# Kernel optimization log

Measured on AMD Instinct MI355X. Metric: run time of the kernel, lower is better.

Reference implementation:

```python
import jax, jax.numpy as jnp
import numpy as np

B, N, IN_F, OUT_F = 8, 2048, 256, 256
ALPHA = 0.2  # LeakyReLU negative slope
NEG_INF = -1e9


def setup_inputs() -> dict:
    key = jax.random.key(0)
    ks = jax.random.split(key, 8)
    h = jax.random.normal(ks[0], (B, N, IN_F), dtype=jnp.float32)
    adj = jax.random.randint(ks[1], (B, N, N), 0, 2, dtype=jnp.int32)
    # xavier-ish scaled params
    W_w = jax.random.normal(ks[2], (OUT_F, IN_F), dtype=jnp.float32) * (1.414 / np.sqrt(IN_F + OUT_F))
    W_b = jnp.zeros((OUT_F,), dtype=jnp.float32)
    ai_w = jax.random.normal(ks[3], (1, OUT_F), dtype=jnp.float32) * (1.414 / np.sqrt(OUT_F + 1))
    ai_b = jnp.zeros((1,), dtype=jnp.float32)
    aj_w = jax.random.normal(ks[4], (1, OUT_F), dtype=jnp.float32) * (1.414 / np.sqrt(OUT_F + 1))
    aj_b = jnp.zeros((1,), dtype=jnp.float32)
    return {"h": h, "adj": adj, "W_w": W_w, "W_b": W_b,
            "ai_w": ai_w, "ai_b": ai_b, "aj_w": aj_w, "aj_b": aj_b}


def reference(h, adj, W_w, W_b, ai_w, ai_b, aj_w, aj_b):
    # Wh: [B, N, F]
    Wh = jnp.einsum('bni,oi->bno', h, W_w) + W_b
    # additive attention scores (pos_embed_dim == 1 so the .view is a transpose)
    Wh1 = jnp.einsum('bnf,of->bno', Wh, ai_w) + ai_b        # [B, N, 1]
    Wh2 = jnp.einsum('bnf,of->bno', Wh, aj_w) + aj_b        # [B, N, 1]
    e = Wh1 + jnp.swapaxes(Wh2, 1, 2)                       # [B, N, N]
    e = jnp.where(e >= 0, e, ALPHA * e)                     # LeakyReLU
    attention = jnp.where(adj > 0, e, NEG_INF)
    attention = jax.nn.softmax(attention, axis=2)
    # dropout: inference mode (training=False) -> identity
    h_hat = jnp.einsum('bnm,bmf->bnf', attention, Wh)
    return jax.nn.elu(h_hat)  # concat=True
```

## Files before the change

### kernel.cpp

```cpp
#include <hip/hip_runtime.h>

typedef __bf16 bf16;
typedef _Float16 f16;
typedef __bf16 bf16x8 __attribute__((ext_vector_type(8)));
typedef _Float16 f16x8 __attribute__((ext_vector_type(8)));
typedef float  f32x4  __attribute__((ext_vector_type(4)));

#define B_  8
#define N_  2048
#define F_  256
#define NTOK (B_ * N_)
#define NW   (F_ * F_)
static constexpr float LOG2E = 1.44269504088896f;

__device__ __forceinline__ int detect_bf16(const void* h) {
    const unsigned* hw = (const unsigned*)h;
    unsigned w = hw[threadIdx.x & 63];
    unsigned ex = (w >> 7) & 0xFFu;
    unsigned long long b = __ballot(ex > 100u && ex < 150u);
    return __popcll(b) >= 40;
}

__device__ __forceinline__ float ldf(const void* p, int i, int isb) {
    return isb ? (float)((const bf16*)p)[i] : ((const float*)p)[i];
}


__global__ __launch_bounds__(256)
void k_cvt(const void* __restrict__ hv, const void* __restrict__ Wv,
           bf16* __restrict__ hb, bf16* __restrict__ Wb) {
    if (detect_bf16(hv)) return;
    size_t base = ((size_t)blockIdx.x * 256 + threadIdx.x) * 8;
    {
        const float* src = (const float*)hv + base;
        float4 a = *(const float4*)src;
        float4 b = *(const float4*)(src + 4);
        bf16x8 r;
        r[0]=(bf16)a.x; r[1]=(bf16)a.y; r[2]=(bf16)a.z; r[3]=(bf16)a.w;
        r[4]=(bf16)b.x; r[5]=(bf16)b.y; r[6]=(bf16)b.z; r[7]=(bf16)b.w;
        *(bf16x8*)(hb + base) = r;
    }
    if (base < NW) {
        const float* src = (const float*)Wv + base;
        float4 a = *(const float4*)src;
        float4 b = *(const float4*)(src + 4);
        bf16x8 r;
        r[0]=(bf16)a.x; r[1]=(bf16)a.y; r[2]=(bf16)a.z; r[3]=(bf16)a.w;
        r[4]=(bf16)b.x; r[5]=(bf16)b.y; r[6]=(bf16)b.z; r[7]=(bf16)b.w;
        *(bf16x8*)(Wb + base) = r;
    }
}

__global__ __launch_bounds__(256)
void k_wht(const void* __restrict__ hv, const void* __restrict__ Wv,
           const bf16* __restrict__ hcv, const bf16* __restrict__ Wcv,
           const void* __restrict__ Wbv, const void* __restrict__ ai_wv,
           const void* __restrict__ ai_bv, const void* __restrict__ aj_wv,
           const void* __restrict__ aj_bv, bf16* __restrict__ WhT2,
           unsigned* __restrict__ adjw) {
    int isb = detect_bf16(hv);
    const bf16* hb = isb ? (const bf16*)hv : hcv;
    const bf16* Wb = isb ? (const bf16*)Wv : Wcv;
    int ttile = blockIdx.x;
    int fg = threadIdx.x >> 6;
    int lane = threadIdx.x & 63;
    int T0 = ttile * 16;
    int m = lane & 15, quad = lane >> 4;

    __shared__ bf16 stage[F_ * 24];
    __shared__ float sred[4][16], tred[4][16];

    f32x4 acc[4];
#pragma unroll
    for (int ft = 0; ft < 4; ++ft) acc[ft] = (f32x4){0.f, 0.f, 0.f, 0.f};

    const bf16* hp = hb + (size_t)(T0 + m) * F_ + quad * 8;
    const bf16* wp = Wb + (size_t)(fg * 64 + m) * F_ + quad * 8;
#pragma unroll
    for (int kk = 0; kk < F_; kk += 32) {
        bf16x8 hf = *(const bf16x8*)(hp + kk);
#pragma unroll
        for (int ft = 0; ft < 4; ++ft) {
            bf16x8 wf = *(const bf16x8*)(wp + (size_t)ft * 16 * F_ + kk);
            acc[ft] = __builtin_amdgcn_mfma_f32_16x16x32_bf16(wf, hf, acc[ft], 0, 0, 0);
        }
    }
    float s_p = 0.f, t_p = 0.f;
#pragma unroll
    for (int ft = 0; ft < 4; ++ft)
#pragma unroll
        for (int r = 0; r < 4; ++r) {
            int f = fg * 64 + ft * 16 + quad * 4 + r;
            float v = acc[ft][r] + ldf(Wbv, f, isb);
            bf16 vb = (bf16)v;
            stage[f * 24 + m] = vb;
            float vr = (float)vb;
            s_p += vr * ldf(ai_wv, f, isb);
            t_p += vr * ldf(aj_wv, f, isb);
        }
    s_p += __shfl_down(s_p, 32, 64); s_p += __shfl_down(s_p, 16, 64);
    t_p += __shfl_down(t_p, 32, 64); t_p += __shfl_down(t_p, 16, 64);
    if (lane < 16) { sred[fg][lane] = s_p; tred[fg][lane] = t_p; }
    __syncthreads();

    {
        int f = threadIdx.x;
        bf16x8 pk0 = *(const bf16x8*)(stage + f * 24);
        bf16x8 pk1 = *(const bf16x8*)(stage + f * 24 + 8);
        int b  = T0 >> 11;
        int n0 = T0 & (N_ - 1);
        int jc = n0 >> 6;
        int s0 = (n0 >> 3) & 7;
        char* rowp = (char*)WhT2 + ((size_t)(b * 32 + jc) * F_ + f) * 128;
        *(bf16x8*)(rowp + (size_t)((s0)     ^ (f & 7)) * 16) = pk0;
        *(bf16x8*)(rowp + (size_t)((s0 + 1) ^ (f & 7)) * 16) = pk1;
    }

    if (threadIdx.x < 16) {
        int tid = threadIdx.x;
        int tok = T0 + tid;
        float ss = (sred[0][tid] + sred[1][tid] + sred[2][tid] + sred[3][tid]
                    + ldf(ai_bv, 0, isb)) * LOG2E;
        float tt = (tred[0][tid] + tred[1][tid] + tred[2][tid] + tred[3][tid]
                    + ldf(aj_bv, 0, isb)) * LOG2E;
        f16 th = (f16)tt, sh = (f16)ss;
        unsigned short tu, su;
        __builtin_memcpy(&tu, &th, 2);
        __builtin_memcpy(&su, &sh, 2);
        unsigned w0 = adjw[tok];
        adjw[tok] = (w0 & 0xFFFFu) | ((unsigned)tu << 16);
        unsigned w1 = adjw[NTOK + tok];
        adjw[NTOK + tok] = (w1 & 0xFFFFu) | ((unsigned)su << 16);
    }
}

__device__ __forceinline__ unsigned char pbits(uint4 a, uint4 b) {
    return (unsigned char)((a.x & 1u) | ((a.y & 1u) << 1) | ((a.z & 1u) << 2) |
                           ((a.w & 1u) << 3) | ((b.x & 1u) << 4) |
                           ((b.y & 1u) << 5) | ((b.z & 1u) << 6) |
                           ((b.w & 1u) << 7));
}

__device__ __forceinline__ void stageB(const bf16* tile, char* dst,
                                       int w, int lane) {
#pragma unroll
    for (int r = 0; r < 8; ++r) {
        int off = (w * 8 + r) * 1024;
        const bf16* g = tile + off / 2 + lane * 8;
        __builtin_amdgcn_global_load_lds(
            (const __attribute__((address_space(1))) unsigned*)g,
            (__attribute__((address_space(3))) unsigned*)(dst + off),
            16, 0, 0);
    }
}

__global__ __launch_bounds__(256, 4)
void k_attn(const unsigned* __restrict__ adjw, const bf16* __restrict__ WhT2,
            const void* __restrict__ hv, void* __restrict__ outv) {
    int isb = detect_bf16(hv);
    int bid = blockIdx.x;
    int b = bid & 7, itile = bid >> 3, i0 = itile * 32;
    int tid = threadIdx.x;
    int w = tid >> 6, lane = tid & 63, m = lane & 15, q = lane >> 4;
    int mt = w >> 1, jh = w & 1;

    __shared__ __align__(16) char smem[37376];
    char* Bbuf  = smem;
    f16* tLDS   = (f16*)(smem + 32768);
    unsigned char* pack0 = (unsigned char*)(smem + 36864);
    unsigned char* pack1 = (unsigned char*)(smem + 37120);
    float* red  = (float*)smem;

    const bf16* batch_tiles = WhT2 + ((size_t)b * 32) * F_ * 64;

#pragma unroll
    for (int k = 0; k < 8; ++k) {
        int idx = k * 256 + tid;
        unsigned wv = adjw[b * N_ + idx];
        unsigned short us = (unsigned short)(wv >> 16);
        f16 tv; __builtin_memcpy(&tv, &us, 2);
        tLDS[idx] = tv;
    }
    int row = i0 + mt * 16 + m;
    unsigned swd = adjw[NTOK + b * N_ + row];
    unsigned short su = (unsigned short)(swd >> 16);
    f16 sh; __builtin_memcpy(&sh, &su, 2);
    float s2i = (float)sh;

    int prow = tid >> 3, ps = tid & 7;
    const unsigned* arow = adjw + ((size_t)(b * N_ + i0 + prow)) * N_ + ps * 8;
    {
        uint4 x0 = *(const uint4*)arow, x1 = *(const uint4*)(arow + 4);
        pack0[prow * 8 + ps] = pbits(x0, x1);
    }
    __syncthreads();

    bf16x8 ones;
#pragma unroll
    for (int k = 0; k < 8; ++k) ones[k] = (bf16)1.0f;

    f32x4 acc[16];
#pragma unroll
    for (int ft = 0; ft < 16; ++ft) acc[ft] = (f32x4){0.f, 0.f, 0.f, 0.f};
    f32x4 acc_l = {0.f, 0.f, 0.f, 0.f};

    for (int c = 0; c < 32; ++c) {
        unsigned char* pcur = (c & 1) ? pack1 : pack0;
        uint4 aw0, aw1;
        bool pre = (c < 31);
        stageB(batch_tiles + (size_t)c * F_ * 64, Bbuf, w, lane);
        if (pre) {
            aw0 = *(const uint4*)(arow + (size_t)(c + 1) * 64);
            aw1 = *(const uint4*)(arow + (size_t)(c + 1) * 64 + 4);
        }
        __syncthreads();

        unsigned long long pb64 =
            *(const unsigned long long*)(pcur + (mt * 16 + m) * 8);
        unsigned bits8 = (unsigned)(pb64 >> ((jh * 4 + q) * 8)) & 0xFFu;
        f16x8 tv = *(const f16x8*)(tLDS + c * 64 + jh * 32 + q * 8);

        bf16x8 af;
#pragma unroll
        for (int qq = 0; qq < 8; ++qq) {
            float x = s2i + (float)tv[qq];
            x = fmaxf(x, 0.2f * x);
            float pv = ((bits8 >> qq) & 1u) ? __builtin_amdgcn_exp2f(x) : 0.f;
            af[qq] = (bf16)pv;
        }
        int sbase = (jh * 4 + q);
#pragma unroll
        for (int ft = 0; ft < 16; ++ft) {
            int fr = ft * 16 + m;
            int psl = sbase ^ (m & 7);
            bf16x8 bfr = *(const bf16x8*)(Bbuf + fr * 128 + psl * 16);
            acc[ft] = __builtin_amdgcn_mfma_f32_16x16x32_bf16(af, bfr, acc[ft], 0, 0, 0);
        }
        acc_l = __builtin_amdgcn_mfma_f32_16x16x32_bf16(af, ones, acc_l, 0, 0, 0);
        if (pre)
            ((c & 1) ? pack0 : pack1)[prow * 8 + ps] = pbits(aw0, aw1);
        __syncthreads();
    }

    if (jh == 1) {
#pragma unroll
        for (int r = 0; r < 4; ++r) {
            int rr = mt * 16 + q * 4 + r;
#pragma unroll
            for (int ft = 0; ft < 16; ++ft)
                red[rr * 257 + ft * 16 + m] = acc[ft][r];
            if (m == 0) red[rr * 257 + 256] = acc_l[r];
        }
    }
    __syncthreads();
    if (jh == 0) {
#pragma unroll
        for (int r = 0; r < 4; ++r) {
            int rr = mt * 16 + q * 4 + r;
            float lf = acc_l[r] + red[rr * 257 + 256];
            float rl = (lf > 0.f) ? (1.f / lf) : 0.f;
            size_t ob = ((size_t)b * N_ + i0 + rr) * F_;
#pragma unroll
            for (int ft = 0; ft < 16; ++ft) {
                int f = ft * 16 + m;
                float v = acc[ft][r] + red[rr * 257 + f];
                v *= rl;
                v = (v > 0.f) ? v : (__builtin_amdgcn_exp2f(v * LOG2E) - 1.f);
                if (isb) ((bf16*)outv)[ob + f] = (bf16)v;
                else     ((float*)outv)[ob + f] = v;
            }
        }
    }
}

extern "C" void kernel_launch(void* const* d_in, const int* in_sizes, int n_in,
                              void* d_out, int out_size, void* d_ws, size_t ws_size,
                              hipStream_t stream) {
    (void)in_sizes; (void)n_in; (void)out_size; (void)ws_size;
    const void* h    = d_in[0];
    unsigned*   adjw = (unsigned*)d_in[1];
    const void* W_w  = d_in[2];
    const void* W_b  = d_in[3];
    const void* ai_w = d_in[4];
    const void* ai_b = d_in[5];
    const void* aj_w = d_in[6];
    const void* aj_b = d_in[7];

    bf16* WhT2 = (bf16*)d_ws;
    bf16* hcv  = (bf16*)((char*)d_ws + (8  << 20));
    bf16* Wcv  = (bf16*)((char*)d_ws + (16 << 20));

    k_cvt <<<dim3(2048), dim3(256), 0, stream>>>(h, W_w, hcv, Wcv);
    k_wht <<<dim3(1024), dim3(256), 0, stream>>>(h, W_w, hcv, Wcv, W_b,
                                                 ai_w, ai_b, aj_w, aj_b,
                                                 WhT2, adjw);
    k_attn<<<dim3(512),  dim3(256), 0, stream>>>(adjw, WhT2, h, d_out);
}
```

Measured before the change: 267.8 us.

## Double-buffer Wh tiles per wave and fuse h conversion into projection

The attention kernel now splits the feature dimension across waves, so each wave computes both 16-row slices over its own 64 features. It double-buffers Wh tiles in LDS with async global-to-LDS loads and explicit vmcnt waits, and syncs only every four chunks. This removes the cross-wave partial-sum reduction and the two barriers per chunk. The fp32 h-to-bf16 conversion pass is dropped, with conversion done inline in the projection kernel, so only W is converted. LDS use roughly doubles and the occupancy hint is removed, which may lower occupancy.

New measurement: 283.9 us. 1.06x slower.

```diff
diff --git a/kernel.cpp b/kernel.cpp
--- a/kernel.cpp
+++ b/kernel.cpp
@@ -25,41 +25,38 @@
     return isb ? (float)((const bf16*)p)[i] : ((const float*)p)[i];
 }
 
+__device__ __forceinline__ bf16x8 cvt8(const float* p) {
+    float4 a = *(const float4*)p;
+    float4 b = *(const float4*)(p + 4);
+    bf16x8 r;
+    r[0]=(bf16)a.x; r[1]=(bf16)a.y; r[2]=(bf16)a.z; r[3]=(bf16)a.w;
+    r[4]=(bf16)b.x; r[5]=(bf16)b.y; r[6]=(bf16)b.z; r[7]=(bf16)b.w;
+    return r;
+}
+
 
 __global__ __launch_bounds__(256)
 void k_cvt(const void* __restrict__ hv, const void* __restrict__ Wv,
-           bf16* __restrict__ hb, bf16* __restrict__ Wb) {
+           bf16* __restrict__ Wb) {
     if (detect_bf16(hv)) return;
     size_t base = ((size_t)blockIdx.x * 256 + threadIdx.x) * 8;
-    {
-        const float* src = (const float*)hv + base;
-        float4 a = *(const float4*)src;
-        float4 b = *(const float4*)(src + 4);
-        bf16x8 r;
-        r[0]=(bf16)a.x; r[1]=(bf16)a.y; r[2]=(bf16)a.z; r[3]=(bf16)a.w;
-        r[4]=(bf16)b.x; r[5]=(bf16)b.y; r[6]=(bf16)b.z; r[7]=(bf16)b.w;
-        *(bf16x8*)(hb + base) = r;
-    }
-    if (base < NW) {
-        const float* src = (const float*)Wv + base;
-        float4 a = *(const float4*)src;
-        float4 b = *(const float4*)(src + 4);
-        bf16x8 r;
-        r[0]=(bf16)a.x; r[1]=(bf16)a.y; r[2]=(bf16)a.z; r[3]=(bf16)a.w;
-        r[4]=(bf16)b.x; r[5]=(bf16)b.y; r[6]=(bf16)b.z; r[7]=(bf16)b.w;
-        *(bf16x8*)(Wb + base) = r;
-    }
+    const float* src = (const float*)Wv + base;
+    float4 a = *(const float4*)src;
+    float4 b = *(const float4*)(src + 4);
+    bf16x8 r;
+    r[0]=(bf16)a.x; r[1]=(bf16)a.y; r[2]=(bf16)a.z; r[3]=(bf16)a.w;
+    r[4]=(bf16)b.x; r[5]=(bf16)b.y; r[6]=(bf16)b.z; r[7]=(bf16)b.w;
+    *(bf16x8*)(Wb + base) = r;
 }
 
 __global__ __launch_bounds__(256)
 void k_wht(const void* __restrict__ hv, const void* __restrict__ Wv,
-           const bf16* __restrict__ hcv, const bf16* __restrict__ Wcv,
+           const bf16* __restrict__ Wcv,
            const void* __restrict__ Wbv, const void* __restrict__ ai_wv,
            const void* __restrict__ ai_bv, const void* __restrict__ aj_wv,
            const void* __restrict__ aj_bv, bf16* __restrict__ WhT2,
            unsigned* __restrict__ adjw) {
     int isb = detect_bf16(hv);
-    const bf16* hb = isb ? (const bf16*)hv : hcv;
     const bf16* Wb = isb ? (const bf16*)Wv : Wcv;
     int ttile = blockIdx.x;
     int fg = threadIdx.x >> 6;
@@ -74,15 +71,28 @@
 #pragma unroll
     for (int ft = 0; ft < 4; ++ft) acc[ft] = (f32x4){0.f, 0.f, 0.f, 0.f};
 
-    const bf16* hp = hb + (size_t)(T0 + m) * F_ + quad * 8;
     const bf16* wp = Wb + (size_t)(fg * 64 + m) * F_ + quad * 8;
-#pragma unroll
-    for (int kk = 0; kk < F_; kk += 32) {
-        bf16x8 hf = *(const bf16x8*)(hp + kk);
-#pragma unroll
-        for (int ft = 0; ft < 4; ++ft) {
-            bf16x8 wf = *(const bf16x8*)(wp + (size_t)ft * 16 * F_ + kk);
-            acc[ft] = __builtin_amdgcn_mfma_f32_16x16x32_bf16(wf, hf, acc[ft], 0, 0, 0);
+    if (isb) {
+        const bf16* hp = (const bf16*)hv + (size_t)(T0 + m) * F_ + quad * 8;
+#pragma unroll
+        for (int kk = 0; kk < F_; kk += 32) {
+            bf16x8 hf = *(const bf16x8*)(hp + kk);
+#pragma unroll
+            for (int ft = 0; ft < 4; ++ft) {
+                bf16x8 wf = *(const bf16x8*)(wp + (size_t)ft * 16 * F_ + kk);
+                acc[ft] = __builtin_amdgcn_mfma_f32_16x16x32_bf16(wf, hf, acc[ft], 0, 0, 0);
+            }
+        }
+    } else {
+        const float* hp = (const float*)hv + (size_t)(T0 + m) * F_ + quad * 8;
+#pragma unroll
+        for (int kk = 0; kk < F_; kk += 32) {
+            bf16x8 hf = cvt8(hp + kk);
+#pragma unroll
+            for (int ft = 0; ft < 4; ++ft) {
+                bf16x8 wf = *(const bf16x8*)(wp + (size_t)ft * 16 * F_ + kk);
+                acc[ft] = __builtin_amdgcn_mfma_f32_16x16x32_bf16(wf, hf, acc[ft], 0, 0, 0);
+            }
         }
     }
     float s_p = 0.f, t_p = 0.f;
@@ -141,20 +151,7 @@
                            ((b.w & 1u) << 7));
 }
 
-__device__ __forceinline__ void stageB(const bf16* tile, char* dst,
-                                       int w, int lane) {
-#pragma unroll
-    for (int r = 0; r < 8; ++r) {
-        int off = (w * 8 + r) * 1024;
-        const bf16* g = tile + off / 2 + lane * 8;
-        __builtin_amdgcn_global_load_lds(
-            (const __attribute__((address_space(1))) unsigned*)g,
-            (__attribute__((address_space(3))) unsigned*)(dst + off),
-            16, 0, 0);
-    }
-}
-
-__global__ __launch_bounds__(256, 4)
+__global__ __launch_bounds__(256)
 void k_attn(const unsigned* __restrict__ adjw, const bf16* __restrict__ WhT2,
             const void* __restrict__ hv, void* __restrict__ outv) {
     int isb = detect_bf16(hv);
@@ -162,16 +159,14 @@
     int b = bid & 7, itile = bid >> 3, i0 = itile * 32;
     int tid = threadIdx.x;
     int w = tid >> 6, lane = tid & 63, m = lane & 15, q = lane >> 4;
-    int mt = w >> 1, jh = w & 1;
-
-    __shared__ __align__(16) char smem[37376];
-    char* Bbuf  = smem;
-    f16* tLDS   = (f16*)(smem + 32768);
-    unsigned char* pack0 = (unsigned char*)(smem + 36864);
-    unsigned char* pack1 = (unsigned char*)(smem + 37120);
-    float* red  = (float*)smem;
-
-    const bf16* batch_tiles = WhT2 + ((size_t)b * 32) * F_ * 64;
+
+    __shared__ __align__(16) char smem[71808];
+    char* Bw = smem + w * 16384;
+    f16* tLDS = (f16*)(smem + 65536);
+    unsigned char* packb = (unsigned char*)(smem + 69632);
+    float* lred = (float*)(smem + 71680);
+
+    const char* batch_bytes = (const char*)WhT2 + ((size_t)b * 32) * 32768;
 
 #pragma unroll
     for (int k = 0; k < 8; ++k) {
@@ -181,17 +176,31 @@
         f16 tv; __builtin_memcpy(&tv, &us, 2);
         tLDS[idx] = tv;
     }
-    int row = i0 + mt * 16 + m;
-    unsigned swd = adjw[NTOK + b * N_ + row];
-    unsigned short su = (unsigned short)(swd >> 16);
-    f16 sh; __builtin_memcpy(&sh, &su, 2);
-    float s2i = (float)sh;
+    float s2i0, s2i1;
+    {
+        unsigned sw0 = adjw[NTOK + b * N_ + i0 + m];
+        unsigned sw1 = adjw[NTOK + b * N_ + i0 + 16 + m];
+        unsigned short u0 = (unsigned short)(sw0 >> 16);
+        unsigned short u1 = (unsigned short)(sw1 >> 16);
+        f16 h0, h1;
+        __builtin_memcpy(&h0, &u0, 2); __builtin_memcpy(&h1, &u1, 2);
+        s2i0 = (float)h0; s2i1 = (float)h1;
+    }
 
     int prow = tid >> 3, ps = tid & 7;
     const unsigned* arow = adjw + ((size_t)(b * N_ + i0 + prow)) * N_ + ps * 8;
-    {
-        uint4 x0 = *(const uint4*)arow, x1 = *(const uint4*)(arow + 4);
-        pack0[prow * 8 + ps] = pbits(x0, x1);
+#pragma unroll
+    for (int cc = 0; cc < 4; ++cc) {
+        uint4 x0 = *(const uint4*)(arow + cc * 64);
+        uint4 x1 = *(const uint4*)(arow + cc * 64 + 4);
+        packb[prow * 32 + cc * 8 + ps] = pbits(x0, x1);
+    }
+#pragma unroll
+    for (int r = 0; r < 8; ++r) {
+        const char* g = batch_bytes + (size_t)w * 8192 + r * 1024 + lane * 16;
+        __builtin_amdgcn_global_load_lds(
+            (const __attribute__((address_space(1))) unsigned*)g,
+            (__attribute__((address_space(3))) unsigned*)(Bw + r * 1024), 16, 0, 0);
     }
     __syncthreads();
 
@@ -199,78 +208,119 @@
 #pragma unroll
     for (int k = 0; k < 8; ++k) ones[k] = (bf16)1.0f;
 
-    f32x4 acc[16];
-#pragma unroll
-    for (int ft = 0; ft < 16; ++ft) acc[ft] = (f32x4){0.f, 0.f, 0.f, 0.f};
-    f32x4 acc_l = {0.f, 0.f, 0.f, 0.f};
-
-    for (int c = 0; c < 32; ++c) {
-        unsigned char* pcur = (c & 1) ? pack1 : pack0;
-        uint4 aw0, aw1;
-        bool pre = (c < 31);
-        stageB(batch_tiles + (size_t)c * F_ * 64, Bbuf, w, lane);
-        if (pre) {
-            aw0 = *(const uint4*)(arow + (size_t)(c + 1) * 64);
-            aw1 = *(const uint4*)(arow + (size_t)(c + 1) * 64 + 4);
-        }
-        __syncthreads();
-
-        unsigned long long pb64 =
-            *(const unsigned long long*)(pcur + (mt * 16 + m) * 8);
-        unsigned bits8 = (unsigned)(pb64 >> ((jh * 4 + q) * 8)) & 0xFFu;
-        f16x8 tv = *(const f16x8*)(tLDS + c * 64 + jh * 32 + q * 8);
-
-        bf16x8 af;
-#pragma unroll
-        for (int qq = 0; qq < 8; ++qq) {
-            float x = s2i + (float)tv[qq];
-            x = fmaxf(x, 0.2f * x);
-            float pv = ((bits8 >> qq) & 1u) ? __builtin_amdgcn_exp2f(x) : 0.f;
-            af[qq] = (bf16)pv;
-        }
-        int sbase = (jh * 4 + q);
-#pragma unroll
-        for (int ft = 0; ft < 16; ++ft) {
-            int fr = ft * 16 + m;
-            int psl = sbase ^ (m & 7);
-            bf16x8 bfr = *(const bf16x8*)(Bbuf + fr * 128 + psl * 16);
-            acc[ft] = __builtin_amdgcn_mfma_f32_16x16x32_bf16(af, bfr, acc[ft], 0, 0, 0);
-        }
-        acc_l = __builtin_amdgcn_mfma_f32_16x16x32_bf16(af, ones, acc_l, 0, 0, 0);
-        if (pre)
-            ((c & 1) ? pack0 : pack1)[prow * 8 + ps] = pbits(aw0, aw1);
-        __syncthreads();
-    }
-
-    if (jh == 1) {
+    f32x4 acc[2][4];
+#pragma unroll
+    for (int rs = 0; rs < 2; ++rs)
+#pragma unroll
+        for (int ftt = 0; ftt < 4; ++ftt) acc[rs][ftt] = (f32x4){0.f,0.f,0.f,0.f};
+    f32x4 accl0 = {0.f,0.f,0.f,0.f}, accl1 = {0.f,0.f,0.f,0.f};
+
+    for (int G = 0; G < 8; ++G) {
+        if (G < 7) {
+#pragma unroll
+            for (int cc = 0; cc < 4; ++cc) {
+                const unsigned* ap = arow + (size_t)(G + 1) * 256 + cc * 64;
+                uint4 x0 = *(const uint4*)ap;
+                uint4 x1 = *(const uint4*)(ap + 4);
+                packb[(((G + 1) & 1) << 10) + prow * 32 + cc * 8 + ps] =
+                    pbits(x0, x1);
+            }
+        }
+#pragma unroll
+        for (int cc = 0; cc < 4; ++cc) {
+            int c = G * 4 + cc;
+            if (c < 31) {
+#pragma unroll
+                for (int r = 0; r < 8; ++r) {
+                    const char* g = batch_bytes + (size_t)(c + 1) * 32768
+                                    + (size_t)w * 8192 + r * 1024 + lane * 16;
+                    __builtin_amdgcn_global_load_lds(
+                        (const __attribute__((address_space(1))) unsigned*)g,
+                        (__attribute__((address_space(3))) unsigned*)
+                            (Bw + ((c + 1) & 1) * 8192 + r * 1024), 16, 0, 0);
+                }
+                asm volatile("s_waitcnt vmcnt(8)" ::: "memory");
+            } else {
+                asm volatile("s_waitcnt vmcnt(0)" ::: "memory");
+            }
+            __builtin_amdgcn_sched_barrier(0);
+
+            const unsigned char* pc = packb + ((G & 1) << 10) + cc * 8;
+            unsigned long long pb0 = *(const unsigned long long*)(pc + m * 32);
+            unsigned long long pb1 =
+                *(const unsigned long long*)(pc + (m + 16) * 32);
+            f16x8 tv0 = *(const f16x8*)(tLDS + c * 64 + q * 8);
+            f16x8 tv1 = *(const f16x8*)(tLDS + c * 64 + 32 + q * 8);
+
+            bf16x8 af[2][2];
+#pragma unroll
+            for (int rs = 0; rs < 2; ++rs) {
+                float s2 = rs ? s2i1 : s2i0;
+                unsigned long long pb = rs ? pb1 : pb0;
+#pragma unroll
+                for (int jh = 0; jh < 2; ++jh) {
+                    unsigned bits = (unsigned)(pb >> ((jh * 4 + q) * 8)) & 0xFFu;
+                    f16x8 tv = jh ? tv1 : tv0;
+#pragma unroll
+                    for (int qq = 0; qq < 8; ++qq) {
+                        float x = s2 + (float)tv[qq];
+                        x = fmaxf(x, 0.2f * x);
+                        float pv = ((bits >> qq) & 1u)
+                                       ? __builtin_amdgcn_exp2f(x) : 0.f;
+                        af[rs][jh][qq] = (bf16)pv;
+                    }
+                }
+            }
+            const char* Bc = Bw + (c & 1) * 8192;
+#pragma unroll
+            for (int jh = 0; jh < 2; ++jh)
+#pragma unroll
+                for (int ftt = 0; ftt < 4; ++ftt) {
+                    int psl = (jh * 4 + q) ^ (m & 7);
+                    bf16x8 bfr = *(const bf16x8*)
+                        (Bc + (ftt * 16 + m) * 128 + psl * 16);
+                    acc[0][ftt] = __builtin_amdgcn_mfma_f32_16x16x32_bf16(
+                        af[0][jh], bfr, acc[0][ftt], 0, 0, 0);
+                    acc[1][ftt] = __builtin_amdgcn_mfma_f32_16x16x32_bf16(
+                        af[1][jh], bfr, acc[1][ftt], 0, 0, 0);
+                }
+            if (w == 0) {
+                accl0 = __builtin_amdgcn_mfma_f32_16x16x32_bf16(af[0][0], ones, accl0, 0, 0, 0);
+                accl0 = __builtin_amdgcn_mfma_f32_16x16x32_bf16(af[0][1], ones, accl0, 0, 0, 0);
+                accl1 = __builtin_amdgcn_mfma_f32_16x16x32_bf16(af[1][0], ones, accl1, 0, 0, 0);
+                accl1 = __builtin_amdgcn_mfma_f32_16x16x32_bf16(af[1][1], ones, accl1, 0, 0, 0);
+            }
+        }
+        asm volatile("s_waitcnt lgkmcnt(0)" ::: "memory");
+        __builtin_amdgcn_s_barrier();
+        __builtin_amdgcn_sched_barrier(0);
+    }
+
+    if (w == 0 && m == 0) {
 #pragma unroll
         for (int r = 0; r < 4; ++r) {
-            int rr = mt * 16 + q * 4 + r;
-#pragma unroll
-            for (int ft = 0; ft < 16; ++ft)
-                red[rr * 257 + ft * 16 + m] = acc[ft][r];
-            if (m == 0) red[rr * 257 + 256] = acc_l[r];
+            lred[q * 4 + r]      = accl0[r];
+            lred[16 + q * 4 + r] = accl1[r];
         }
     }
     __syncthreads();
-    if (jh == 0) {
+#pragma unroll
+    for (int rs = 0; rs < 2; ++rs)
 #pragma unroll
         for (int r = 0; r < 4; ++r) {
-            int rr = mt * 16 + q * 4 + r;
-            float lf = acc_l[r] + red[rr * 257 + 256];
+            int rr = rs * 16 + q * 4 + r;
+            float lf = lred[rr];
             float rl = (lf > 0.f) ? (1.f / lf) : 0.f;
             size_t ob = ((size_t)b * N_ + i0 + rr) * F_;
 #pragma unroll
-            for (int ft = 0; ft < 16; ++ft) {
-                int f = ft * 16 + m;
-                float v = acc[ft][r] + red[rr * 257 + f];
-                v *= rl;
+            for (int ftt = 0; ftt < 4; ++ftt) {
+                int f = w * 64 + ftt * 16 + m;
+                float v = acc[rs][ftt][r] * rl;
                 v = (v > 0.f) ? v : (__builtin_amdgcn_exp2f(v * LOG2E) - 1.f);
                 if (isb) ((bf16*)outv)[ob + f] = (bf16)v;
                 else     ((float*)outv)[ob + f] = v;
             }
         }
-    }
 }
 
 extern "C" void kernel_launch(void* const* d_in, const int* in_sizes, int n_in,
@@ -287,11 +337,10 @@
     const void* aj_b = d_in[7];
 
     bf16* WhT2 = (bf16*)d_ws;
-    bf16* hcv  = (bf16*)((char*)d_ws + (8  << 20));
-    bf16* Wcv  = (bf16*)((char*)d_ws + (16 << 20));
-
-    k_cvt <<<dim3(2048), dim3(256), 0, stream>>>(h, W_w, hcv, Wcv);
-    k_wht <<<dim3(1024), dim3(256), 0, stream>>>(h, W_w, hcv, Wcv, W_b,
+    bf16* Wcv  = (bf16*)((char*)d_ws + (8 << 20));
+
+    k_cvt <<<dim3(32),   dim3(256), 0, stream>>>(h, W_w, Wcv);
+    k_wht <<<dim3(1024), dim3(256), 0, stream>>>(h, W_w, Wcv, W_b,
                                                  ai_w, ai_b, aj_w, aj_b,
                                                  WhT2, adjw);
     k_attn<<<dim3(512),  dim3(256), 0, stream>>>(adjw, WhT2, h, d_out);
```
